# Optimization experiments

Measured on AMD Instinct MI355X. Metric: run time of the kernel, lower is better.

Reference implementation:

```python
import jax, jax.numpy as jnp
import numpy as np

B, L, HID, H, FF = 32, 1024, 512, 8, 2048
DH = HID // H  # head_dim = 64; deterministic FAVOR features => M == DH
KEPS = 1e-3    # performer kernel_epsilon
LN_EPS = 1e-6  # flax LayerNorm default


def setup_inputs() -> dict:
    key = jax.random.key(0)
    ks = jax.random.split(key, 12)
    sa = 1.0 / np.sqrt(HID)
    sf = 1.0 / np.sqrt(FF)
    return {
        "x": jax.random.normal(ks[0], (B, L, HID), jnp.float32),
        "Wq": jax.random.normal(ks[1], (HID, H, DH), jnp.float32) * sa,
        "bq": jnp.zeros((H, DH), jnp.float32),
        "Wk": jax.random.normal(ks[2], (HID, H, DH), jnp.float32) * sa,
        "bk": jnp.zeros((H, DH), jnp.float32),
        "Wv": jax.random.normal(ks[3], (HID, H, DH), jnp.float32) * sa,
        "bv": jnp.zeros((H, DH), jnp.float32),
        "Wo": jax.random.normal(ks[4], (H, DH, HID), jnp.float32) * sa,
        "bo": jnp.zeros((HID,), jnp.float32),
        "ln1_scale": jnp.ones((HID,), jnp.float32),
        "ln1_bias": jnp.zeros((HID,), jnp.float32),
        "W1": jax.random.normal(ks[5], (HID, FF), jnp.float32) * sa,
        "b1": jnp.zeros((FF,), jnp.float32),
        "W2": jax.random.normal(ks[6], (FF, HID), jnp.float32) * sf,
        "b2": jnp.zeros((HID,), jnp.float32),
        "ln2_scale": jnp.ones((HID,), jnp.float32),
        "ln2_bias": jnp.zeros((HID,), jnp.float32),
    }


def _layernorm(x, scale, bias):
    mu = jnp.mean(x, axis=-1, keepdims=True)
    var = jnp.mean(jnp.square(x - mu), axis=-1, keepdims=True)
    return (x - mu) * jax.lax.rsqrt(var + LN_EPS) * scale + bias


def _favor_bidirectional(q, k, v):
    # Performer generalized attention, deterministic features:
    # phi(x) = relu(x) + kernel_epsilon, renormalized.
    qp = jax.nn.relu(q) + KEPS  # [B,L,H,M]
    kp = jax.nn.relu(k) + KEPS  # [B,L,H,M]
    kv = jnp.einsum('blhm,blhd->bhmd', kp, v)        # [B,H,M,D]
    num = jnp.einsum('blhm,bhmd->blhd', qp, kv)      # [B,L,H,D]
    den = jnp.einsum('blhm,bhm->blh', qp, kp.sum(axis=1))  # [B,L,H]
    return num / den[..., None]


def reference(x, Wq, bq, Wk, bk, Wv, bv, Wo, bo,
              ln1_scale, ln1_bias, W1, b1, W2, b2, ln2_scale, ln2_bias):
    # Multi-head projections (flax MHA DenseGeneral layout [HID,H,DH])
    q = jnp.einsum('blc,chd->blhd', x, Wq) + bq
    k = jnp.einsum('blc,chd->blhd', x, Wk) + bk
    v = jnp.einsum('blc,chd->blhd', x, Wv) + bv
    attn = _favor_bidirectional(q, k, v)                  # [B,L,H,DH]
    attended = jnp.einsum('blhd,hdc->blc', attn, Wo) + bo # [B,L,HID]
    h = _layernorm(attended + x, ln1_scale, ln1_bias)
    ff = jax.nn.relu(h @ W1 + b1) @ W2 + b2
    return _layernorm(ff + h, ln2_scale, ln2_bias)
```

## Files before the change

### kernel.cpp

```cpp
#include <hip/hip_runtime.h>


#define DI __device__ __forceinline__
#define AS1 __attribute__((address_space(1)))
#define AS3 __attribute__((address_space(3)))
#define GLD16(g, l) __builtin_amdgcn_global_load_lds((const AS1 void*)(g), (AS3 void*)(l), 16, 0, 0)

typedef __attribute__((ext_vector_type(8))) short bf16x8;
typedef __attribute__((ext_vector_type(4))) float f32x4;

DI float b2f(short s){ unsigned int u = ((unsigned int)(unsigned short)s) << 16; float f; __builtin_memcpy(&f, &u, 4); return f; }
DI short f2b(float f){ unsigned int u; __builtin_memcpy(&u, &f, 4); u += 0x7fffu + ((u >> 16) & 1u); return (short)(u >> 16); }

constexpr int Ll = 1024;
constexpr int SPLIT = 16384;

__global__ __launch_bounds__(256) void k_cvt_x(const float* __restrict__ x, short* __restrict__ xb){
  long i = (long)blockIdx.x * 256 + threadIdx.x;
  const float4* p = (const float4*)x + i * 2;
  float4 a = p[0], b = p[1];
  bf16x8 o;
  o[0]=f2b(a.x); o[1]=f2b(a.y); o[2]=f2b(a.z); o[3]=f2b(a.w);
  o[4]=f2b(b.x); o[5]=f2b(b.y); o[6]=f2b(b.z); o[7]=f2b(b.w);
  *((bf16x8*)xb + i) = o;
}

__global__ void k_tcvt(const float* __restrict__ in, short* __restrict__ out, int R, int C){
  __shared__ float t[32][33];
  int c0 = blockIdx.x * 32, r0 = blockIdx.y * 32;
  int x = threadIdx.x, y = threadIdx.y;
  #pragma unroll
  for (int j = 0; j < 4; ++j) t[y + 8*j][x] = in[(long)(r0 + y + 8*j) * C + c0 + x];
  __syncthreads();
  #pragma unroll
  for (int j = 0; j < 4; ++j) out[(long)(c0 + y + 8*j) * R + r0 + x] = f2b(t[x][y + 8*j]);
}

__global__ void k_tcvt4(const float* __restrict__ s0, const float* __restrict__ s1,
                        const float* __restrict__ s2, const float* __restrict__ s3,
                        short* __restrict__ d0, short* __restrict__ d1,
                        short* __restrict__ d2, short* __restrict__ d3){
  __shared__ float t[32][33];
  int z = blockIdx.z;
  const float* in = z == 0 ? s0 : z == 1 ? s1 : z == 2 ? s2 : s3;
  short* out      = z == 0 ? d0 : z == 1 ? d1 : z == 2 ? d2 : d3;
  int c0 = blockIdx.x * 32, r0 = blockIdx.y * 32;
  int x = threadIdx.x, y = threadIdx.y;
  #pragma unroll
  for (int j = 0; j < 4; ++j) t[y + 8*j][x] = in[(long)(r0 + y + 8*j) * 512 + c0 + x];
  __syncthreads();
  #pragma unroll
  for (int j = 0; j < 4; ++j) out[(long)(c0 + y + 8*j) * 512 + r0 + x] = f2b(t[x][y + 8*j]);
}

__global__ void k_pack_bias(const float* __restrict__ bq, const float* __restrict__ bk,
                            const float* __restrict__ bv, float* __restrict__ bqkv){
  int i = blockIdx.x * 256 + threadIdx.x;
  if (i < 512) bqkv[i] = bq[i];
  else if (i < 1024) bqkv[i] = bk[i - 512];
  else if (i < 1536) bqkv[i] = bv[i - 1024];
}

template<int EPI, int KD>
__global__ __launch_bounds__(512, 2) void k_gemm256(
    const short* __restrict__ A0, const short* __restrict__ A1,
    const short* __restrict__ BT, int NT,
    const float* __restrict__ bias, const short* __restrict__ residX,
    short* __restrict__ oQ, short* __restrict__ oK, short* __restrict__ oV,
    short* __restrict__ o1)
{
  __shared__ short lds[65536];
  const int tid = threadIdx.x;
  const int w = tid >> 6, lane = tid & 63;
  const int wm = w >> 2, wn = w & 3;
  const int lg = lane >> 4, lr = lane & 15;
  const int lrow = lane >> 3, lslot = (lane & 7) ^ lrow;

  const int per = gridDim.x >> 3;
  const int wg = (blockIdx.x & 7) * per + (blockIdx.x >> 3);
  const long m0 = (long)(wg / NT) * 256, n0 = (long)(wg % NT) * 256;

  const short* Ause = A0;
  long mbase = m0;
  if (A1 != A0 && m0 >= SPLIT) { Ause = A1; mbase = m0 - SPLIT; }

  f32x4 acc[8][4];
  #pragma unroll
  for (int i = 0; i < 8; ++i)
    #pragma unroll
    for (int j = 0; j < 4; ++j) acc[i][j] = 0.f;

  auto stage_all = [&](int buf, int k0){
    #pragma unroll
    for (int half = 0; half < 2; ++half)
      #pragma unroll
      for (int q = 0; q < 2; ++q) {
        int r = w * 16 + q * 8;
        GLD16(Ause + (mbase + half * 128 + r + lrow) * KD + k0 + lslot * 8,
              (char*)lds + (buf * 16384 + half * 8192 + r * 64) * 2);
        GLD16(BT + (n0 + half * 128 + r + lrow) * KD + k0 + lslot * 8,
              (char*)lds + (32768 + buf * 16384 + half * 8192 + r * 64) * 2);
      }
  };

  constexpr int NKT = KD / 64;
  stage_all(0, 0);
  stage_all(1, 64);

  for (int kt = 0; kt < NKT; ++kt) {
    const int cur = kt & 1;
    if (kt + 1 < NKT) { asm volatile("s_waitcnt vmcnt(8)" ::: "memory"); }
    else              { asm volatile("s_waitcnt vmcnt(0)" ::: "memory"); }
    __builtin_amdgcn_s_barrier();

    const char* Ab = (const char*)lds + (cur * 16384 + wm * 8192) * 2;
    const char* Bb = (const char*)lds + (32768 + cur * 16384 + (wn >> 1) * 8192) * 2;

    bf16x8 fB[2][2][2];
    #pragma unroll
    for (int qc = 0; qc < 2; ++qc)
      #pragma unroll
      for (int j = 0; j < 2; ++j)
        #pragma unroll
        for (int kk = 0; kk < 2; ++kk) {
          int rb = (wn & 1) * 64 + qc * 32 + j * 16 + lr;
          fB[qc][j][kk] = *(const bf16x8*)(Bb + rb * 128 + ((kk * 64 + lg * 16) ^ ((rb & 7) << 4)));
        }
    #pragma unroll
    for (int qr = 0; qr < 2; ++qr) {
      bf16x8 fA[4][2];
      #pragma unroll
      for (int i = 0; i < 4; ++i)
        #pragma unroll
        for (int kk = 0; kk < 2; ++kk) {
          int ra = qr * 64 + i * 16 + lr;
          fA[i][kk] = *(const bf16x8*)(Ab + ra * 128 + ((kk * 64 + lg * 16) ^ ((ra & 7) << 4)));
        }
      __builtin_amdgcn_s_setprio(1);
      #pragma unroll
      for (int i = 0; i < 4; ++i)
        #pragma unroll
        for (int qc = 0; qc < 2; ++qc)
          #pragma unroll
          for (int j = 0; j < 2; ++j)
            #pragma unroll
            for (int kk = 0; kk < 2; ++kk)
              acc[qr * 4 + i][qc * 2 + j] =
                __builtin_amdgcn_mfma_f32_16x16x32_bf16(fA[i][kk], fB[qc][j][kk], acc[qr * 4 + i][qc * 2 + j], 0, 0, 0);
      __builtin_amdgcn_s_setprio(0);
    }

    __builtin_amdgcn_s_barrier();
    if (kt + 2 < NKT) stage_all(cur, (kt + 2) * 64);
  }

  #pragma unroll
  for (int fr = 0; fr < 8; ++fr)
    #pragma unroll
    for (int fc = 0; fc < 4; ++fc)
      #pragma unroll
      for (int r = 0; r < 4; ++r) {
        int grow = (int)m0 + wm * 128 + fr * 16 + lg * 4 + r;
        int gcol = (int)n0 + wn * 64 + fc * 16 + lr;
        float v = acc[fr][fc][r];
        if constexpr (EPI == 0) {
          v += bias[gcol];
          int which = gcol >> 9, hd = gcol & 511, h = hd >> 6, d = hd & 63;
          int b = grow >> 10, l = grow & 1023;
          long o = ((long)(b * 8 + h) * 1024 + l) * 64 + d;
          if (which == 2) oV[o] = f2b(v);
          else { float p = fmaxf(v, 0.f) + 1e-3f; if (which) oK[o] = f2b(p); else oQ[o] = f2b(p); }
        } else if constexpr (EPI == 1) {
          v += bias[gcol] + b2f(residX[(long)grow * 512 + gcol]);
          oQ[(long)grow * 512 + gcol] = f2b(v);
        } else if constexpr (EPI == 2) {
          v = fmaxf(v + bias[gcol], 0.f);
          if (grow < SPLIT) oQ[(long)grow * 2048 + gcol] = f2b(v);
          else              o1[(long)(grow - SPLIT) * 2048 + gcol] = f2b(v);
        } else {
          long idx = (long)grow * 512 + gcol;
          v += bias[gcol] + b2f(oQ[idx]);
          oQ[idx] = f2b(v);
        }
      }
}

__global__ __launch_bounds__(256) void k_fkv_part(const short* __restrict__ kp, const short* __restrict__ vb,
                                                  float* __restrict__ kvp, float* __restrict__ ksp)
{
  constexpr int LS = 72;
  __shared__ short kps[64 * LS];
  __shared__ short vps[64 * LS];
  int bh = blockIdx.x & 255, c = blockIdx.x >> 8;
  const short* kpp = kp + (long)bh * Ll * 64;
  const short* vpp = vb + (long)bh * Ll * 64;
  int tid = threadIdx.x;
  int mb = (tid & 15) * 4, db = (tid >> 4) * 4;
  float acc[4][4];
  float ks[4] = {0.f, 0.f, 0.f, 0.f};
  #pragma unroll
  for (int i = 0; i < 4; ++i)
    #pragma unroll
    for (int j = 0; j < 4; ++j) acc[i][j] = 0.f;

  for (int l0 = c * 256; l0 < c * 256 + 256; l0 += 64) {
    __syncthreads();
    #pragma unroll
    for (int s = 0; s < 2; ++s) {
      int idx = tid + s * 256;
      int row = idx >> 3, c8 = idx & 7;
      *(bf16x8*)(&kps[row * LS + c8 * 8]) = *(const bf16x8*)(kpp + (long)(l0 + row) * 64 + c8 * 8);
      *(bf16x8*)(&vps[row * LS + c8 * 8]) = *(const bf16x8*)(vpp + (long)(l0 + row) * 64 + c8 * 8);
    }
    __syncthreads();
    #pragma unroll 4
    for (int l = 0; l < 64; ++l) {
      short4 ka = *(const short4*)(&kps[l * LS + mb]);
      short4 va = *(const short4*)(&vps[l * LS + db]);
      float kf[4] = {b2f(ka.x), b2f(ka.y), b2f(ka.z), b2f(ka.w)};
      float vf[4] = {b2f(va.x), b2f(va.y), b2f(va.z), b2f(va.w)};
      if (tid < 16) { ks[0] += kf[0]; ks[1] += kf[1]; ks[2] += kf[2]; ks[3] += kf[3]; }
      #pragma unroll
      for (int i = 0; i < 4; ++i)
        #pragma unroll
        for (int j = 0; j < 4; ++j) acc[i][j] += kf[i] * vf[j];
    }
  }
  float* kout = kvp + (long)c * 1048576 + (long)bh * 4096;
  #pragma unroll
  for (int i = 0; i < 4; ++i)
    #pragma unroll
    for (int j = 0; j < 4; ++j)
      kout[(db + j) * 64 + mb + i] = acc[i][j];
  if (tid < 16) {
    #pragma unroll
    for (int i = 0; i < 4; ++i) ksp[(long)c * 16384 + bh * 64 + mb + i] = ks[i];
  }
}

__global__ __launch_bounds__(256) void k_fkv_reduce(const float* __restrict__ kvp, const float* __restrict__ ksp,
                                                    short* __restrict__ kvt, float* __restrict__ ksum)
{
  int g = blockIdx.x * 256 + threadIdx.x;
  float s = kvp[g] + kvp[g + 1048576] + kvp[g + 2 * 1048576] + kvp[g + 3 * 1048576];
  kvt[g] = f2b(s);
  if (g < 16384)
    ksum[g] = ksp[g] + ksp[g + 16384] + ksp[g + 2 * 16384] + ksp[g + 3 * 16384];
}

__global__ __launch_bounds__(256) void k_favor_num(const short* __restrict__ qp, const short* __restrict__ kvt,
                                                   const float* __restrict__ ksum, short* __restrict__ attn)
{
  constexpr int LS = 72;
  __shared__ short Qs[128 * 64];
  __shared__ short kvs[64 * LS];
  __shared__ float part[256];
  __shared__ float den[128];
  int bh = blockIdx.x >> 3, lt = blockIdx.x & 7;
  int b = bh >> 3, h = bh & 7;
  const short* qpp = qp + ((long)bh * Ll + lt * 128) * 64;
  int tid = threadIdx.x;
  int wave = tid >> 6, lane = tid & 63;
  int lrow = lane >> 3, lslot = (lane & 7) ^ lrow;

  #pragma unroll
  for (int s = 0; s < 4; ++s) {
    int rs = (s * 4 + wave) * 8;
    GLD16(qpp + (long)(rs + lrow) * 64 + lslot * 8, &Qs[rs * 64]);
  }
  #pragma unroll
  for (int s = 0; s < 2; ++s) {
    int idx = tid + s * 256;
    int row = idx >> 3, c8 = idx & 7;
    *(bf16x8*)(&kvs[row * LS + c8 * 8]) = *(const bf16x8*)(kvt + (long)bh * 4096 + row * 64 + c8 * 8);
  }
  __syncthreads();
  {
    int r = tid >> 1, half = tid & 1;
    const float* kss = ksum + bh * 64 + half * 32;
    float s = 0.f;
    #pragma unroll
    for (int c = 0; c < 4; ++c) {
      int cc = half * 4 + c;
      bf16x8 v = *(const bf16x8*)((const char*)Qs + r * 128 + ((cc * 16) ^ ((r & 7) << 4)));
      #pragma unroll
      for (int j = 0; j < 8; ++j) s += b2f(v[j]) * kss[c * 8 + j];
    }
    part[tid] = s;
  }
  __syncthreads();
  if (tid < 128) den[tid] = part[2 * tid] + part[2 * tid + 1];
  __syncthreads();

  int wr = wave >> 1, wc = wave & 1;
  int lg = lane >> 4, lr = lane & 15;
  f32x4 acc[4][2];
  #pragma unroll
  for (int i = 0; i < 4; ++i) { acc[i][0] = 0.f; acc[i][1] = 0.f; }
  #pragma unroll
  for (int kk = 0; kk < 2; ++kk) {
    bf16x8 af[4], bfr[2];
    #pragma unroll
    for (int i = 0; i < 4; ++i) {
      int ra = wr * 64 + i * 16 + lr;
      af[i] = *(const bf16x8*)((const char*)Qs + ra * 128 + ((kk * 64 + lg * 16) ^ ((ra & 7) << 4)));
    }
    #pragma unroll
    for (int j = 0; j < 2; ++j)
      bfr[j] = *(const bf16x8*)(&kvs[(wc * 32 + j * 16 + lr) * LS + kk * 32 + lg * 8]);
    #pragma unroll
    for (int i = 0; i < 4; ++i)
      #pragma unroll
      for (int j = 0; j < 2; ++j)
        acc[i][j] = __builtin_amdgcn_mfma_f32_16x16x32_bf16(af[i], bfr[j], acc[i][j], 0, 0, 0);
  }
  #pragma unroll
  for (int i = 0; i < 4; ++i)
    #pragma unroll
    for (int j = 0; j < 2; ++j)
      #pragma unroll
      for (int r = 0; r < 4; ++r) {
        int rl = wr * 64 + i * 16 + lg * 4 + r;
        int d  = wc * 32 + j * 16 + lr;
        int t  = b * Ll + lt * 128 + rl;
        attn[(long)t * 512 + h * 64 + d] = f2b(acc[i][j][r] / den[rl]);
      }
}

__global__ __launch_bounds__(256) void k_ln_bb(const short* __restrict__ in, const float* __restrict__ sc,
                                               const float* __restrict__ bi, short* __restrict__ ob)
{
  int row = blockIdx.x * 4 + (threadIdx.x >> 6);
  int lane = threadIdx.x & 63;
  bf16x8 v = *((const bf16x8*)(in + (long)row * 512) + lane);
  float e[8];
  #pragma unroll
  for (int j = 0; j < 8; ++j) e[j] = b2f(v[j]);
  float s = 0.f, s2 = 0.f;
  #pragma unroll
  for (int j = 0; j < 8; ++j) { s += e[j]; s2 += e[j] * e[j]; }
  #pragma unroll
  for (int off = 32; off; off >>= 1) { s += __shfl_xor(s, off); s2 += __shfl_xor(s2, off); }
  float mu = s * (1.f / 512.f);
  float var = s2 * (1.f / 512.f) - mu * mu;
  float rstd = rsqrtf(var + 1e-6f);
  int c0 = lane * 8;
  bf16x8 o;
  #pragma unroll
  for (int j = 0; j < 8; ++j) o[j] = f2b((e[j] - mu) * rstd * sc[c0 + j] + bi[c0 + j]);
  *((bf16x8*)(ob + (long)row * 512) + lane) = o;
}

__global__ __launch_bounds__(256) void k_ln_bf(const short* __restrict__ in, const float* __restrict__ sc,
                                               const float* __restrict__ bi, float* __restrict__ of)
{
  int row = blockIdx.x * 4 + (threadIdx.x >> 6);
  int lane = threadIdx.x & 63;
  bf16x8 v = *((const bf16x8*)(in + (long)row * 512) + lane);
  float e[8];
  #pragma unroll
  for (int j = 0; j < 8; ++j) e[j] = b2f(v[j]);
  float s = 0.f, s2 = 0.f;
  #pragma unroll
  for (int j = 0; j < 8; ++j) { s += e[j]; s2 += e[j] * e[j]; }
  #pragma unroll
  for (int off = 32; off; off >>= 1) { s += __shfl_xor(s, off); s2 += __shfl_xor(s2, off); }
  float mu = s * (1.f / 512.f);
  float var = s2 * (1.f / 512.f) - mu * mu;
  float rstd = rsqrtf(var + 1e-6f);
  int c0 = lane * 8;
  float o0[4], o1[4];
  #pragma unroll
  for (int j = 0; j < 4; ++j) {
    o0[j] = (e[j]     - mu) * rstd * sc[c0 + j]     + bi[c0 + j];
    o1[j] = (e[4 + j] - mu) * rstd * sc[c0 + 4 + j] + bi[c0 + 4 + j];
  }
  *(float4*)(of + (long)row * 512 + c0)     = (float4){o0[0], o0[1], o0[2], o0[3]};
  *(float4*)(of + (long)row * 512 + c0 + 4) = (float4){o1[0], o1[1], o1[2], o1[3]};
}

extern "C" void kernel_launch(void* const* d_in, const int* in_sizes, int n_in,
                              void* d_out, int out_size, void* d_ws, size_t ws_size,
                              hipStream_t stream)
{
  const float* x   = (const float*)d_in[0];
  const float* Wq  = (const float*)d_in[1];
  const float* bq  = (const float*)d_in[2];
  const float* Wk  = (const float*)d_in[3];
  const float* bk  = (const float*)d_in[4];
  const float* Wv  = (const float*)d_in[5];
  const float* bv  = (const float*)d_in[6];
  const float* Wo  = (const float*)d_in[7];
  const float* bo  = (const float*)d_in[8];
  const float* g1  = (const float*)d_in[9];
  const float* be1 = (const float*)d_in[10];
  const float* W1  = (const float*)d_in[11];
  const float* b1  = (const float*)d_in[12];
  const float* W2  = (const float*)d_in[13];
  const float* b2  = (const float*)d_in[14];
  const float* g2  = (const float*)d_in[15];
  const float* be2 = (const float*)d_in[16];
  float* out = (float*)d_out;

  const long MB = 1024L * 1024L;
  char* ws = (char*)d_ws;
  short* qp    = (short*)(ws + 0 * MB);
  short* kp    = (short*)(ws + 32 * MB);
  short* vb    = (short*)(ws + 64 * MB);
  short* attn  = (short*)(ws + 32 * MB);
  short* hb    = (short*)(ws + 0 * MB);
  short* hpreB = (short*)(ws + 64 * MB);
  short* ffa0  = (short*)(ws + 32 * MB);
  short* wqkvT = (short*)(ws + 96 * MB);
  short* woT   = (short*)(ws + 98 * MB);
  short* w1T   = (short*)(ws + 99 * MB);
  short* w2T   = (short*)(ws + 101 * MB);
  short* kvt   = (short*)(ws + 103 * MB);
  float* ksum  = (float*)(ws + 105 * MB);
  float* bqkv  = (float*)(ws + 105 * MB + 65536);

  short* xb   = (short*)d_out;
  float* kvp  = (float*)((char*)d_out + 32 * MB);
  float* ksp  = (float*)((char*)d_out + 48 * MB);
  short* ffa1 = (short*)d_out;

  dim3 tb(32, 8);
  k_cvt_x<<<8192, 256, 0, stream>>>(x, xb);
  k_tcvt4<<<dim3(16, 16, 4), tb, 0, stream>>>(Wq, Wk, Wv, Wo,
      wqkvT, wqkvT + 512 * 512, wqkvT + 1024 * 512, woT);
  k_tcvt<<<dim3(64, 16), tb, 0, stream>>>(W1, w1T, 512, 2048);
  k_tcvt<<<dim3(16, 64), tb, 0, stream>>>(W2, w2T, 2048, 512);
  k_pack_bias<<<6, 256, 0, stream>>>(bq, bk, bv, bqkv);

  k_gemm256<0, 512><<<768, 512, 0, stream>>>(xb, xb, wqkvT, 6, bqkv, nullptr, qp, kp, vb, nullptr);
  k_fkv_part<<<1024, 256, 0, stream>>>(kp, vb, kvp, ksp);
  k_fkv_reduce<<<4096, 256, 0, stream>>>(kvp, ksp, kvt, ksum);
  k_favor_num<<<2048, 256, 0, stream>>>(qp, kvt, ksum, attn);
  k_gemm256<1, 512><<<256, 512, 0, stream>>>(attn, attn, woT, 2, bo, xb, hpreB, nullptr, nullptr, nullptr);
  k_ln_bb<<<8192, 256, 0, stream>>>(hpreB, g1, be1, hb);
  k_gemm256<2, 512><<<1024, 512, 0, stream>>>(hb, hb, w1T, 8, b1, nullptr, ffa0, nullptr, nullptr, ffa1);
  k_gemm256<3, 2048><<<256, 512, 0, stream>>>(ffa0, ffa1, w2T, 2, b2, nullptr, hb, nullptr, nullptr, nullptr);
  k_ln_bf<<<8192, 256, 0, stream>>>(hb, g2, be2, out);
}
```

Before: 367.6 us.

## Restructure GEMM main loop into fine-grained 8-phase ping-pong schedule

Replaces the simple double-buffered k-loop with an unrolled two-tile schedule split into eight phases, each pairing LDS fragment reads and staging of half-tiles for A/B with a quarter of the MFMA work, separated by barriers. Global-to-LDS loads are interleaved at a finer grain with vmcnt(4) gates, so memory traffic overlaps compute more continuously. The cost is many more barriers per k-tile and tighter ordering constraints; correctness depends on the buffer reuse ordering being exactly right.

```diff
diff --git a/kernel.cpp b/kernel.cpp
--- a/kernel.cpp
+++ b/kernel.cpp
@@ -90,69 +90,95 @@
     #pragma unroll
     for (int j = 0; j < 4; ++j) acc[i][j] = 0.f;
 
-  auto stage_all = [&](int buf, int k0){
-    #pragma unroll
-    for (int half = 0; half < 2; ++half)
-      #pragma unroll
-      for (int q = 0; q < 2; ++q) {
-        int r = w * 16 + q * 8;
-        GLD16(Ause + (mbase + half * 128 + r + lrow) * KD + k0 + lslot * 8,
-              (char*)lds + (buf * 16384 + half * 8192 + r * 64) * 2);
-        GLD16(BT + (n0 + half * 128 + r + lrow) * KD + k0 + lslot * 8,
-              (char*)lds + (32768 + buf * 16384 + half * 8192 + r * 64) * 2);
-      }
-  };
+  const char* Abase = (const char*)lds + wm * 16384;
+  const char* Bbase = (const char*)lds + 65536 + (wn >> 1) * 16384;
+
+#define STAGE_A(buf, half, t) do {                                              \
+    int k0_ = (t) * 64;                                                         \
+    _Pragma("unroll")                                                           \
+    for (int q_ = 0; q_ < 2; ++q_) {                                            \
+      int rs_ = w * 16 + q_ * 8;                                                \
+      GLD16(Ause + (mbase + (half) * 128 + rs_ + lrow) * KD + k0_ + lslot * 8,  \
+            (char*)lds + ((buf) * 16384 + (half) * 8192 + rs_ * 64) * 2);       \
+    } } while (0)
+#define STAGE_B(buf, half, t) do {                                              \
+    int k0_ = (t) * 64;                                                         \
+    _Pragma("unroll")                                                           \
+    for (int q_ = 0; q_ < 2; ++q_) {                                            \
+      int rs_ = w * 16 + q_ * 8;                                                \
+      GLD16(BT + (n0 + (half) * 128 + rs_ + lrow) * KD + k0_ + lslot * 8,       \
+            (char*)lds + (32768 + (buf) * 16384 + (half) * 8192 + rs_ * 64) * 2); \
+    } } while (0)
+#define READ_A(buf, qr) do {                                                    \
+    _Pragma("unroll")                                                           \
+    for (int i_ = 0; i_ < 4; ++i_)                                              \
+      _Pragma("unroll")                                                         \
+      for (int kk_ = 0; kk_ < 2; ++kk_) {                                       \
+        int ra_ = (qr) * 64 + i_ * 16 + lr;                                     \
+        fA[i_][kk_] = *(const bf16x8*)(Abase + (buf) * 32768 + ra_ * 128 +      \
+                       ((kk_ * 64 + lg * 16) ^ ((ra_ & 7) << 4)));              \
+      } } while (0)
+#define READ_B(FB, buf, qc) do {                                                \
+    _Pragma("unroll")                                                           \
+    for (int j_ = 0; j_ < 2; ++j_)                                              \
+      _Pragma("unroll")                                                         \
+      for (int kk_ = 0; kk_ < 2; ++kk_) {                                       \
+        int rb_ = (wn & 1) * 64 + (qc) * 32 + j_ * 16 + lr;                     \
+        FB[j_][kk_] = *(const bf16x8*)(Bbase + (buf) * 32768 + rb_ * 128 +      \
+                       ((kk_ * 64 + lg * 16) ^ ((rb_ & 7) << 4)));              \
+      } } while (0)
+#define MFMA_Q(qr, qc, FB) do {                                                 \
+    __builtin_amdgcn_s_setprio(1);                                              \
+    _Pragma("unroll")                                                           \
+    for (int i_ = 0; i_ < 4; ++i_)                                              \
+      _Pragma("unroll")                                                         \
+      for (int j_ = 0; j_ < 2; ++j_)                                            \
+        _Pragma("unroll")                                                       \
+        for (int kk_ = 0; kk_ < 2; ++kk_)                                       \
+          acc[(qr)*4+i_][(qc)*2+j_] = __builtin_amdgcn_mfma_f32_16x16x32_bf16(  \
+              fA[i_][kk_], FB[j_][kk_], acc[(qr)*4+i_][(qc)*2+j_], 0, 0, 0);    \
+    __builtin_amdgcn_s_setprio(0);                                              \
+  } while (0)
+#define BARR __builtin_amdgcn_s_barrier()
+#define GATEC asm volatile("s_waitcnt vmcnt(4)" ::: "memory")
+#define GATE0 asm volatile("s_waitcnt vmcnt(0)" ::: "memory")
 
   constexpr int NKT = KD / 64;
-  stage_all(0, 0);
-  stage_all(1, 64);
-
-  for (int kt = 0; kt < NKT; ++kt) {
-    const int cur = kt & 1;
-    if (kt + 1 < NKT) { asm volatile("s_waitcnt vmcnt(8)" ::: "memory"); }
-    else              { asm volatile("s_waitcnt vmcnt(0)" ::: "memory"); }
-    __builtin_amdgcn_s_barrier();
-
-    const char* Ab = (const char*)lds + (cur * 16384 + wm * 8192) * 2;
-    const char* Bb = (const char*)lds + (32768 + cur * 16384 + (wn >> 1) * 8192) * 2;
-
-    bf16x8 fB[2][2][2];
-    #pragma unroll
-    for (int qc = 0; qc < 2; ++qc)
-      #pragma unroll
-      for (int j = 0; j < 2; ++j)
-        #pragma unroll
-        for (int kk = 0; kk < 2; ++kk) {
-          int rb = (wn & 1) * 64 + qc * 32 + j * 16 + lr;
-          fB[qc][j][kk] = *(const bf16x8*)(Bb + rb * 128 + ((kk * 64 + lg * 16) ^ ((rb & 7) << 4)));
-        }
-    #pragma unroll
-    for (int qr = 0; qr < 2; ++qr) {
-      bf16x8 fA[4][2];
-      #pragma unroll
-      for (int i = 0; i < 4; ++i)
-        #pragma unroll
-        for (int kk = 0; kk < 2; ++kk) {
-          int ra = qr * 64 + i * 16 + lr;
-          fA[i][kk] = *(const bf16x8*)(Ab + ra * 128 + ((kk * 64 + lg * 16) ^ ((ra & 7) << 4)));
-        }
-      __builtin_amdgcn_s_setprio(1);
-      #pragma unroll
-      for (int i = 0; i < 4; ++i)
-        #pragma unroll
-        for (int qc = 0; qc < 2; ++qc)
-          #pragma unroll
-          for (int j = 0; j < 2; ++j)
-            #pragma unroll
-            for (int kk = 0; kk < 2; ++kk)
-              acc[qr * 4 + i][qc * 2 + j] =
-                __builtin_amdgcn_mfma_f32_16x16x32_bf16(fA[i][kk], fB[qc][j][kk], acc[qr * 4 + i][qc * 2 + j], 0, 0, 0);
-      __builtin_amdgcn_s_setprio(0);
-    }
-
-    __builtin_amdgcn_s_barrier();
-    if (kt + 2 < NKT) stage_all(cur, (kt + 2) * 64);
-  }
+  bf16x8 fA[4][2], fB0[2][2], fB1[2][2];
+
+  STAGE_A(0, 0, 0); STAGE_A(0, 1, 0); STAGE_B(0, 0, 0); STAGE_B(0, 1, 0);
+  STAGE_B(1, 0, 1); STAGE_B(1, 1, 1);
+  GATEC; BARR;
+
+  for (int it = 0; it < NKT / 2; ++it) {
+    const int t0 = 2 * it, t1 = 2 * it + 1;
+    const bool s0 = (t0 + 2 < NKT), s1 = (t1 + 2 < NKT);
+    READ_A(0, 0); READ_B(fB0, 0, 0); STAGE_A(1, 0, t1);
+    BARR; MFMA_Q(0, 0, fB0); BARR;
+    READ_B(fB1, 0, 1); STAGE_A(1, 1, t1);
+    BARR; MFMA_Q(0, 1, fB1); BARR;
+    READ_A(0, 1); if (s0) STAGE_B(0, 0, t0 + 2);
+    BARR; MFMA_Q(1, 0, fB0); BARR;
+    if (s0) { STAGE_B(0, 1, t0 + 2); GATEC; } else { GATE0; }
+    BARR; MFMA_Q(1, 1, fB1); BARR;
+    READ_A(1, 0); READ_B(fB0, 1, 0); if (s0) STAGE_A(0, 0, t0 + 2);
+    BARR; MFMA_Q(0, 0, fB0); BARR;
+    READ_B(fB1, 1, 1); if (s0) STAGE_A(0, 1, t0 + 2);
+    BARR; MFMA_Q(0, 1, fB1); BARR;
+    READ_A(1, 1); if (s1) STAGE_B(1, 0, t1 + 2);
+    BARR; MFMA_Q(1, 0, fB0); BARR;
+    if (s1) { STAGE_B(1, 1, t1 + 2); GATEC; } else { GATE0; }
+    BARR; MFMA_Q(1, 1, fB1); BARR;
+  }
+
+#undef STAGE_A
+#undef STAGE_B
+#undef READ_A
+#undef READ_B
+#undef MFMA_Q
+#undef BARR
+#undef GATEC
+#undef GATE0
 
   #pragma unroll
   for (int fr = 0; fr < 8; ++fr)
```

Result: no change. 365.8 us (-0.5%).

## Switch GEMM to 32x32x16 MFMA, simplify pipeline, fuse prep kernels

Applied to the files above, without the earlier changes.

Moves the 256x256 GEMM from 16x16x32 to 32x32x16 bf16 MFMA tiles, using f32x16 accumulators and a new epilogue index mapping. The aim is fewer LDS fragment loads per MFMA and higher MFMA throughput. The LDS pipeline changes from two stages prefetched ahead with explicit vmcnt waits to a single prefetch issued after a __syncthreads, which may expose more load latency. The five prep kernels (x conversion, weight transposes, bias pack) are merged into one launch to cut launch overhead.

```diff
diff --git a/kernel.cpp b/kernel.cpp
--- a/kernel.cpp
+++ b/kernel.cpp
@@ -8,6 +8,7 @@
 
 typedef __attribute__((ext_vector_type(8))) short bf16x8;
 typedef __attribute__((ext_vector_type(4))) float f32x4;
+typedef __attribute__((ext_vector_type(16))) float f32x16;
 
 DI float b2f(short s){ unsigned int u = ((unsigned int)(unsigned short)s) << 16; float f; __builtin_memcpy(&f, &u, 4); return f; }
 DI short f2b(float f){ unsigned int u; __builtin_memcpy(&u, &f, 4); u += 0x7fffu + ((u >> 16) & 1u); return (short)(u >> 16); }
@@ -15,47 +16,52 @@
 constexpr int Ll = 1024;
 constexpr int SPLIT = 16384;
 
-__global__ __launch_bounds__(256) void k_cvt_x(const float* __restrict__ x, short* __restrict__ xb){
-  long i = (long)blockIdx.x * 256 + threadIdx.x;
-  const float4* p = (const float4*)x + i * 2;
-  float4 a = p[0], b = p[1];
-  bf16x8 o;
-  o[0]=f2b(a.x); o[1]=f2b(a.y); o[2]=f2b(a.z); o[3]=f2b(a.w);
-  o[4]=f2b(b.x); o[5]=f2b(b.y); o[6]=f2b(b.z); o[7]=f2b(b.w);
-  *((bf16x8*)xb + i) = o;
-}
-
-__global__ void k_tcvt(const float* __restrict__ in, short* __restrict__ out, int R, int C){
-  __shared__ float t[32][33];
-  int c0 = blockIdx.x * 32, r0 = blockIdx.y * 32;
-  int x = threadIdx.x, y = threadIdx.y;
-  #pragma unroll
-  for (int j = 0; j < 4; ++j) t[y + 8*j][x] = in[(long)(r0 + y + 8*j) * C + c0 + x];
-  __syncthreads();
-  #pragma unroll
-  for (int j = 0; j < 4; ++j) out[(long)(c0 + y + 8*j) * R + r0 + x] = f2b(t[x][y + 8*j]);
-}
-
-__global__ void k_tcvt4(const float* __restrict__ s0, const float* __restrict__ s1,
-                        const float* __restrict__ s2, const float* __restrict__ s3,
-                        short* __restrict__ d0, short* __restrict__ d1,
-                        short* __restrict__ d2, short* __restrict__ d3){
-  __shared__ float t[32][33];
-  int z = blockIdx.z;
-  const float* in = z == 0 ? s0 : z == 1 ? s1 : z == 2 ? s2 : s3;
-  short* out      = z == 0 ? d0 : z == 1 ? d1 : z == 2 ? d2 : d3;
-  int c0 = blockIdx.x * 32, r0 = blockIdx.y * 32;
-  int x = threadIdx.x, y = threadIdx.y;
-  #pragma unroll
-  for (int j = 0; j < 4; ++j) t[y + 8*j][x] = in[(long)(r0 + y + 8*j) * 512 + c0 + x];
-  __syncthreads();
-  #pragma unroll
-  for (int j = 0; j < 4; ++j) out[(long)(c0 + y + 8*j) * 512 + r0 + x] = f2b(t[x][y + 8*j]);
-}
-
-__global__ void k_pack_bias(const float* __restrict__ bq, const float* __restrict__ bk,
-                            const float* __restrict__ bv, float* __restrict__ bqkv){
-  int i = blockIdx.x * 256 + threadIdx.x;
+__global__ __launch_bounds__(256) void k_prep(
+    const float* __restrict__ x, short* __restrict__ xb,
+    const float* __restrict__ Wq, const float* __restrict__ Wk,
+    const float* __restrict__ Wv, const float* __restrict__ Wo,
+    short* __restrict__ wqkvT, short* __restrict__ woT,
+    const float* __restrict__ W1, short* __restrict__ w1T,
+    const float* __restrict__ W2, short* __restrict__ w2T,
+    const float* __restrict__ bq, const float* __restrict__ bk,
+    const float* __restrict__ bv, float* __restrict__ bqkv)
+{
+  int bid = blockIdx.x;
+  if (bid < 8192) {
+    long i = (long)bid * 256 + threadIdx.x;
+    const float4* p = (const float4*)x + i * 2;
+    float4 a = p[0], b = p[1];
+    bf16x8 o;
+    o[0]=f2b(a.x); o[1]=f2b(a.y); o[2]=f2b(a.z); o[3]=f2b(a.w);
+    o[4]=f2b(b.x); o[5]=f2b(b.y); o[6]=f2b(b.z); o[7]=f2b(b.w);
+    *((bf16x8*)xb + i) = o;
+    return;
+  }
+  bid -= 8192;
+  if (bid < 3072) {
+    __shared__ float t[32][33];
+    const float* in; short* out; int R, C, bx, by;
+    if (bid < 1024) {
+      int z = bid >> 8, ti = bid & 255;
+      bx = ti & 15; by = ti >> 4; R = 512; C = 512;
+      in  = z == 0 ? Wq : z == 1 ? Wk : z == 2 ? Wv : Wo;
+      out = z == 0 ? wqkvT : z == 1 ? wqkvT + 512 * 512 : z == 2 ? wqkvT + 1024 * 512 : woT;
+    } else if (bid < 2048) {
+      int ti = bid - 1024; bx = ti & 63; by = ti >> 6; R = 512; C = 2048; in = W1; out = w1T;
+    } else {
+      int ti = bid - 2048; bx = ti & 15; by = ti >> 4; R = 2048; C = 512; in = W2; out = w2T;
+    }
+    int c0 = bx * 32, r0 = by * 32;
+    int xx = threadIdx.x & 31, yy = threadIdx.x >> 5;
+    #pragma unroll
+    for (int j = 0; j < 4; ++j) t[yy + 8*j][xx] = in[(long)(r0 + yy + 8*j) * C + c0 + xx];
+    __syncthreads();
+    #pragma unroll
+    for (int j = 0; j < 4; ++j) out[(long)(c0 + yy + 8*j) * R + r0 + xx] = f2b(t[xx][yy + 8*j]);
+    return;
+  }
+  bid -= 3072;
+  int i = bid * 256 + threadIdx.x;
   if (i < 512) bqkv[i] = bq[i];
   else if (i < 1024) bqkv[i] = bk[i - 512];
   else if (i < 1536) bqkv[i] = bv[i - 1024];
@@ -73,7 +79,7 @@
   const int tid = threadIdx.x;
   const int w = tid >> 6, lane = tid & 63;
   const int wm = w >> 2, wn = w & 3;
-  const int lg = lane >> 4, lr = lane & 15;
+  const int l31 = lane & 31, g16 = (lane >> 5) * 16;
   const int lrow = lane >> 3, lslot = (lane & 7) ^ lrow;
 
   const int per = gridDim.x >> 3;
@@ -84,11 +90,11 @@
   long mbase = m0;
   if (A1 != A0 && m0 >= SPLIT) { Ause = A1; mbase = m0 - SPLIT; }
 
-  f32x4 acc[8][4];
-  #pragma unroll
-  for (int i = 0; i < 8; ++i)
-    #pragma unroll
-    for (int j = 0; j < 4; ++j) acc[i][j] = 0.f;
+  f32x16 acc[4][2];
+  #pragma unroll
+  for (int i = 0; i < 4; ++i)
+    #pragma unroll
+    for (int j = 0; j < 2; ++j) acc[i][j] = 0.f;
 
   auto stage_all = [&](int buf, int k0){
     #pragma unroll
@@ -105,64 +111,49 @@
 
   constexpr int NKT = KD / 64;
   stage_all(0, 0);
-  stage_all(1, 64);
 
   for (int kt = 0; kt < NKT; ++kt) {
     const int cur = kt & 1;
-    if (kt + 1 < NKT) { asm volatile("s_waitcnt vmcnt(8)" ::: "memory"); }
-    else              { asm volatile("s_waitcnt vmcnt(0)" ::: "memory"); }
-    __builtin_amdgcn_s_barrier();
+    __syncthreads();
+    if (kt + 1 < NKT) stage_all(cur ^ 1, (kt + 1) * 64);
 
     const char* Ab = (const char*)lds + (cur * 16384 + wm * 8192) * 2;
     const char* Bb = (const char*)lds + (32768 + cur * 16384 + (wn >> 1) * 8192) * 2;
 
-    bf16x8 fB[2][2][2];
-    #pragma unroll
-    for (int qc = 0; qc < 2; ++qc)
-      #pragma unroll
-      for (int j = 0; j < 2; ++j)
+    bf16x8 fB[2][4];
+    #pragma unroll
+    for (int cg = 0; cg < 2; ++cg)
+      #pragma unroll
+      for (int ks = 0; ks < 4; ++ks) {
+        int rb = (wn & 1) * 64 + cg * 32 + l31;
+        fB[cg][ks] = *(const bf16x8*)(Bb + rb * 128 + ((ks * 32 + g16) ^ ((rb & 7) << 4)));
+      }
+    #pragma unroll
+    for (int rg = 0; rg < 4; ++rg) {
+      bf16x8 fA[4];
+      int ra = rg * 32 + l31;
+      #pragma unroll
+      for (int ks = 0; ks < 4; ++ks)
+        fA[ks] = *(const bf16x8*)(Ab + ra * 128 + ((ks * 32 + g16) ^ ((ra & 7) << 4)));
+      __builtin_amdgcn_s_setprio(1);
+      #pragma unroll
+      for (int cg = 0; cg < 2; ++cg)
         #pragma unroll
-        for (int kk = 0; kk < 2; ++kk) {
-          int rb = (wn & 1) * 64 + qc * 32 + j * 16 + lr;
-          fB[qc][j][kk] = *(const bf16x8*)(Bb + rb * 128 + ((kk * 64 + lg * 16) ^ ((rb & 7) << 4)));
-        }
-    #pragma unroll
-    for (int qr = 0; qr < 2; ++qr) {
-      bf16x8 fA[4][2];
-      #pragma unroll
-      for (int i = 0; i < 4; ++i)
-        #pragma unroll
-        for (int kk = 0; kk < 2; ++kk) {
-          int ra = qr * 64 + i * 16 + lr;
-          fA[i][kk] = *(const bf16x8*)(Ab + ra * 128 + ((kk * 64 + lg * 16) ^ ((ra & 7) << 4)));
-        }
-      __builtin_amdgcn_s_setprio(1);
-      #pragma unroll
-      for (int i = 0; i < 4; ++i)
-        #pragma unroll
-        for (int qc = 0; qc < 2; ++qc)
-          #pragma unroll
-          for (int j = 0; j < 2; ++j)
-            #pragma unroll
-            for (int kk = 0; kk < 2; ++kk)
-              acc[qr * 4 + i][qc * 2 + j] =
-                __builtin_amdgcn_mfma_f32_16x16x32_bf16(fA[i][kk], fB[qc][j][kk], acc[qr * 4 + i][qc * 2 + j], 0, 0, 0);
+        for (int ks = 0; ks < 4; ++ks)
+          acc[rg][cg] = __builtin_amdgcn_mfma_f32_32x32x16_bf16(fA[ks], fB[cg][ks], acc[rg][cg], 0, 0, 0);
       __builtin_amdgcn_s_setprio(0);
     }
-
-    __builtin_amdgcn_s_barrier();
-    if (kt + 2 < NKT) stage_all(cur, (kt + 2) * 64);
-  }
-
-  #pragma unroll
-  for (int fr = 0; fr < 8; ++fr)
-    #pragma unroll
-    for (int fc = 0; fc < 4; ++fc)
-      #pragma unroll
-      for (int r = 0; r < 4; ++r) {
-        int grow = (int)m0 + wm * 128 + fr * 16 + lg * 4 + r;
-        int gcol = (int)n0 + wn * 64 + fc * 16 + lr;
-        float v = acc[fr][fc][r];
+  }
+
+  #pragma unroll
+  for (int rg = 0; rg < 4; ++rg)
+    #pragma unroll
+    for (int cg = 0; cg < 2; ++cg)
+      #pragma unroll
+      for (int reg = 0; reg < 16; ++reg) {
+        int grow = (int)m0 + wm * 128 + rg * 32 + (reg & 3) + 8 * (reg >> 2) + ((lane >> 5) << 2);
+        int gcol = (int)n0 + wn * 64 + cg * 32 + l31;
+        float v = acc[rg][cg][reg];
         if constexpr (EPI == 0) {
           v += bias[gcol];
           int which = gcol >> 9, hd = gcol & 511, h = hd >> 6, d = hd & 63;
@@ -424,13 +415,8 @@
   float* ksp  = (float*)((char*)d_out + 48 * MB);
   short* ffa1 = (short*)d_out;
 
-  dim3 tb(32, 8);
-  k_cvt_x<<<8192, 256, 0, stream>>>(x, xb);
-  k_tcvt4<<<dim3(16, 16, 4), tb, 0, stream>>>(Wq, Wk, Wv, Wo,
-      wqkvT, wqkvT + 512 * 512, wqkvT + 1024 * 512, woT);
-  k_tcvt<<<dim3(64, 16), tb, 0, stream>>>(W1, w1T, 512, 2048);
-  k_tcvt<<<dim3(16, 64), tb, 0, stream>>>(W2, w2T, 2048, 512);
-  k_pack_bias<<<6, 256, 0, stream>>>(bq, bk, bv, bqkv);
+  k_prep<<<11270, 256, 0, stream>>>(x, xb, Wq, Wk, Wv, Wo, wqkvT, woT,
+                                    W1, w1T, W2, w2T, bq, bk, bv, bqkv);
 
   k_gemm256<0, 512><<<768, 512, 0, stream>>>(xb, xb, wqkvT, 6, bqkv, nullptr, qp, kp, vb, nullptr);
   k_fkv_part<<<1024, 256, 0, stream>>>(kp, vb, kvp, ksp);
```

Result: slower. 378.0 us (+2.8%).
